# Performance work log

Hardware: AMD Instinct MI355X
Metric: run time of the kernel (lower is better)

## Reference

```python
import jax, jax.numpy as jnp
import numpy as np

B, S, DM, H, DK, DV = 2, 2048, 1024, 16, 64, 64

def setup_inputs() -> dict:
    key = jax.random.key(0)
    ks = jax.random.split(key, 12)
    s = 0.02
    return {
        "Q": jax.random.normal(ks[0], (B, S, DM), jnp.float32),
        "K": jax.random.normal(ks[1], (B, S, DM), jnp.float32),
        "V": jax.random.normal(ks[2], (B, S, DM), jnp.float32),
        "mask": jax.random.randint(ks[3], (B, S, S), 0, 2).astype(bool),
        "wq": jax.random.normal(ks[4], (DM, H * DK), jnp.float32) * s,
        "bq": jnp.zeros((H * DK,), jnp.float32),
        "wk": jax.random.normal(ks[5], (DM, H * DK), jnp.float32) * s,
        "bk": jnp.zeros((H * DK,), jnp.float32),
        "wv": jax.random.normal(ks[6], (DM, H * DV), jnp.float32) * s,
        "bv": jnp.zeros((H * DV,), jnp.float32),
        "wo": jax.random.normal(ks[7], (H * DV, DM), jnp.float32) * s,
        "bo": jnp.zeros((DM,), jnp.float32),
    }

def reference(Q, K, V, mask, wq, bq, wk, bk, wv, bv, wo, bo):
    b = Q.shape[0]
    # projections -> [b, h, s, d]
    q = (Q @ wq + bq).reshape(b, -1, H, DK).transpose(0, 2, 1, 3)
    k = (K @ wk + bk).reshape(b, -1, H, DK).transpose(0, 2, 1, 3)
    v = (V @ wv + bv).reshape(b, -1, H, DV).transpose(0, 2, 1, 3)
    # scaled dot-product attention with boolean mask (True = masked out)
    scores = jnp.einsum("bhqd,bhkd->bhqk", q, k) / jnp.sqrt(jnp.float32(DK))
    scores = jnp.where(mask[:, None, :, :], jnp.float32(-1e9), scores)
    attn = jax.nn.softmax(scores, axis=-1)  # [b,h,s,s]
    ctx = jnp.einsum("bhqk,bhkd->bhqd", attn, v)
    ctx = ctx.transpose(0, 2, 1, 3).reshape(b, -1, H * DV)
    out = ctx @ wo + bo  # [b, s, d_model]
    return out, attn
```

## Files before the change

### kernel.cpp

```cpp
#include <hip/hip_runtime.h>

typedef unsigned short u16;
typedef unsigned int u32;
typedef unsigned long long u64;
typedef __attribute__((ext_vector_type(8))) short bf16x8;
typedef __attribute__((ext_vector_type(4))) float f32x4;

#define NB 2
#define NS 2048
#define NDM 1024
#define NH 16

#define MFMA_B16(a, b, c) __builtin_amdgcn_mfma_f32_16x16x32_bf16(a, b, c, 0, 0, 0)

__device__ __forceinline__ u16 f2bf(float f) {
  union { float f; unsigned u; } v; v.f = f;
  return (u16)((v.u + 0x7fffu + ((v.u >> 16) & 1u)) >> 16);
}

__global__ __launch_bounds__(256) void cast_bf16(const float* __restrict__ in,
                                                 u16* __restrict__ out, int n4) {
  int i = blockIdx.x * 256 + threadIdx.x;
  if (i < n4) {
    const float4 v = reinterpret_cast<const float4*>(in)[i];
    ushort4 o; o.x = f2bf(v.x); o.y = f2bf(v.y); o.z = f2bf(v.z); o.w = f2bf(v.w);
    reinterpret_cast<ushort4*>(out)[i] = o;
  }
}

__global__ __launch_bounds__(256) void transpose_w(const float* __restrict__ in,
                                                   u16* __restrict__ out) {
  __shared__ float tile[32][33];
  int bx = blockIdx.x, by = blockIdx.y;
  int x = threadIdx.x & 31, y0 = threadIdx.x >> 5;
#pragma unroll
  for (int i = 0; i < 4; i++) {
    int y = y0 + i * 8;
    tile[y][x] = in[(by * 32 + y) * NDM + bx * 32 + x];
  }
  __syncthreads();
#pragma unroll
  for (int i = 0; i < 4; i++) {
    int y = y0 + i * 8;
    out[(bx * 32 + y) * NDM + by * 32 + x] = f2bf(tile[x][y]);
  }
}

__global__ __launch_bounds__(256) void mask2bits(const u32* __restrict__ mask, u32* __restrict__ mb) {
  int idx = blockIdx.x * 256 + threadIdx.x;
  u32 mw0 = mask[threadIdx.x & 63];
  bool floatmode = (__ballot(mw0 == 0x3F800000u) != 0ull);
  bool bytemode = !floatmode && (__ballot((mw0 >> 8) != 0u) != 0ull);
  int row = idx >> 6;
  int wword = idx & 63;
  u32 bits = 0;
  if (!bytemode) {
    const uint4* p = reinterpret_cast<const uint4*>(mask + (size_t)row * 2048 + wword * 32);
#pragma unroll
    for (int i = 0; i < 8; i++) {
      uint4 v = p[i];
      bits |= (v.x ? 1u : 0u) << (i * 4 + 0);
      bits |= (v.y ? 1u : 0u) << (i * 4 + 1);
      bits |= (v.z ? 1u : 0u) << (i * 4 + 2);
      bits |= (v.w ? 1u : 0u) << (i * 4 + 3);
    }
  } else {
    const uint4* p = reinterpret_cast<const uint4*>(
        reinterpret_cast<const unsigned char*>(mask) + (size_t)row * 2048 + wword * 32);
#pragma unroll
    for (int i = 0; i < 2; i++) {
      uint4 v = p[i];
      u32 wsv[4] = {v.x, v.y, v.z, v.w};
#pragma unroll
      for (int j = 0; j < 4; j++)
#pragma unroll
        for (int kq = 0; kq < 4; kq++)
          bits |= ((((wsv[j] >> (kq * 8)) & 0xffu) != 0u) ? 1u : 0u) << (i * 16 + j * 4 + kq);
    }
  }
  mb[idx] = bits;
}

struct GArgs { const u16* X; const u16* W; const float* bias; void* out; int mode; float scale; };

__global__ __launch_bounds__(256, 2) void gemm_bt(GArgs g0, GArgs g1, GArgs g2) {
  GArgs ga = (blockIdx.z == 0) ? g0 : (blockIdx.z == 1 ? g1 : g2);
  const int K = 1024, N = 1024;
  __shared__ u16 As[128 * 32];
  __shared__ u16 Bs[128 * 32];
  const int t = threadIdx.x, w = t >> 6, l = t & 63;
  const int m0 = blockIdx.x * 128, n0 = blockIdx.y * 128;
  const int wm = (w >> 1) * 64, wn = (w & 1) * 64;
  const f32x4 fz = {0.f, 0.f, 0.f, 0.f};
  f32x4 acc[4][4];
#pragma unroll
  for (int i = 0; i < 4; i++)
#pragma unroll
    for (int j = 0; j < 4; j++) acc[i][j] = fz;

  for (int k0 = 0; k0 < K; k0 += 32) {
#pragma unroll
    for (int i = 0; i < 2; i++) {
      int idx = i * 256 + w * 64 + l;
      int r = idx >> 2, c = (idx & 3) * 8;
      __builtin_amdgcn_global_load_lds(
          reinterpret_cast<const unsigned*>(ga.X + (size_t)(m0 + r) * K + k0 + c),
          reinterpret_cast<unsigned*>(&As[(i * 256 + w * 64) * 8]), 16, 0, 0);
      __builtin_amdgcn_global_load_lds(
          reinterpret_cast<const unsigned*>(ga.W + (size_t)(n0 + r) * K + k0 + c),
          reinterpret_cast<unsigned*>(&Bs[(i * 256 + w * 64) * 8]), 16, 0, 0);
    }
    __syncthreads();
    bf16x8 af[4], bfr[4];
#pragma unroll
    for (int mt = 0; mt < 4; mt++)
      af[mt] = *reinterpret_cast<const bf16x8*>(&As[(wm + mt * 16 + (l & 15)) * 32 + (l >> 4) * 8]);
#pragma unroll
    for (int nt = 0; nt < 4; nt++)
      bfr[nt] = *reinterpret_cast<const bf16x8*>(&Bs[(wn + nt * 16 + (l & 15)) * 32 + (l >> 4) * 8]);
#pragma unroll
    for (int mt = 0; mt < 4; mt++)
#pragma unroll
      for (int nt = 0; nt < 4; nt++)
        acc[mt][nt] = MFMA_B16(af[mt], bfr[nt], acc[mt][nt]);
    __syncthreads();
  }

#pragma unroll
  for (int nt = 0; nt < 4; nt++) {
    int n = n0 + wn + nt * 16 + (l & 15);
    float bias = ga.bias[n];
#pragma unroll
    for (int mt = 0; mt < 4; mt++) {
      int mb = m0 + wm + mt * 16 + ((l >> 4) << 2);
#pragma unroll
      for (int r = 0; r < 4; r++) {
        int m = mb + r;
        float v = (acc[mt][nt][r] + bias) * ga.scale;
        if (ga.mode == 2) {
          reinterpret_cast<float*>(ga.out)[(size_t)m * N + n] = v;
        } else {
          int b = m >> 11, s = m & 2047, h = n >> 6, d = n & 63;
          if (ga.mode == 0)
            reinterpret_cast<u16*>(ga.out)[(((size_t)(b * NH + h) * NS + s) << 6) + d] = f2bf(v);
          else
            reinterpret_cast<u16*>(ga.out)[((size_t)(b * NH + h) * 64 + d) * NS + s] = f2bf(v);
        }
      }
    }
  }
}

__global__ __launch_bounds__(256, 4) void attn_kernel(
    const u16* __restrict__ qh, const u16* __restrict__ kh, const u16* __restrict__ vT,
    const u32* __restrict__ mb, float* __restrict__ attn, u16* __restrict__ ctx) {
  __shared__ u16 Ks[2][32 * 64];
  __shared__ u16 Vs[2][64 * 32];
  __shared__ u16 Ps[4][16 * 40];
  __shared__ float Pf[4][16 * 36];
  const int tid = threadIdx.x, w = tid >> 6, l = tid & 63;
  int id = blockIdx.x;
  int wgid = (id & 7) * 128 + (id >> 3);
  int qt = wgid & 31, pr = wgid >> 5;
  int h = pr & 15, b = pr >> 4;
  const size_t head = (size_t)b * NH + h;
  const u16* qp = qh + head * NS * 64;
  const u16* kp = kh + head * NS * 64;
  const u16* vp = vT + head * 64 * NS;
  const int qr0 = qt * 64 + w * 16;
  const int lo = l & 15, hi = l >> 4;
  const int rbase = hi << 2;
  const f32x4 fz = {0.f, 0.f, 0.f, 0.f};

  bf16x8 aq0, aq1;
  {
    const u16* p = qp + (size_t)(qr0 + lo) * 64 + hi * 8;
    aq0 = *reinterpret_cast<const bf16x8*>(p);
    aq1 = *reinterpret_cast<const bf16x8*>(p + 32);
  }
  const u32* mrow = mb + ((size_t)b * NS + qr0 + rbase) * 64;

  const int k_row = tid >> 3, k_slot = tid & 7;
  const u16* ksrc0 = kp + (size_t)k_row * 64 + ((k_slot ^ (k_row & 7)) * 8);
  const int v_dv = tid >> 2, v_slot = tid & 3;
  const u16* vsrc0 = vp + (size_t)v_dv * NS + ((v_slot ^ ((v_dv >> 1) & 3)) * 8);

  const int sxk = lo & 7;
  const int sxv = (lo >> 1) & 3;

  float rs0 = 0.f, rs1 = 0.f, rs2 = 0.f, rs3 = 0.f;

  __builtin_amdgcn_global_load_lds(reinterpret_cast<const unsigned*>(ksrc0),
                                   reinterpret_cast<unsigned*>(&Ks[0][w * 512]), 16, 0, 0);
  asm volatile("s_waitcnt vmcnt(0)" ::: "memory");
  __builtin_amdgcn_s_barrier();
  asm volatile("" ::: "memory");

  for (int t = 0; t < 64; ++t) {
    const u16* kbase = &Ks[t & 1][0];
    u16* kdst = &Ks[(t + 1) & 1][w * 512];
    __builtin_amdgcn_global_load_lds(
        reinterpret_cast<const unsigned*>(ksrc0 + (size_t)(t + 1) * 2048),
        reinterpret_cast<unsigned*>(kdst), 16, 0, 0);
    asm volatile("" ::: "memory");
    u32 m0 = mrow[t], m1 = mrow[64 + t], m2 = mrow[128 + t], m3 = mrow[192 + t];
    bf16x8 b00 = *reinterpret_cast<const bf16x8*>(&kbase[(lo) * 64 + ((hi ^ sxk) * 8)]);
    bf16x8 b01 = *reinterpret_cast<const bf16x8*>(&kbase[(lo) * 64 + (((4 + hi) ^ sxk) * 8)]);
    bf16x8 b10 = *reinterpret_cast<const bf16x8*>(&kbase[(16 + lo) * 64 + ((hi ^ sxk) * 8)]);
    bf16x8 b11 = *reinterpret_cast<const bf16x8*>(&kbase[(16 + lo) * 64 + (((4 + hi) ^ sxk) * 8)]);
    f32x4 s0 = MFMA_B16(aq1, b01, MFMA_B16(aq0, b00, fz));
    f32x4 s1 = MFMA_B16(aq1, b11, MFMA_B16(aq0, b10, fz));
    rs0 += ((m0 >> lo) & 1u) ? 0.f : __expf(s0[0]);
    rs1 += ((m1 >> lo) & 1u) ? 0.f : __expf(s0[1]);
    rs2 += ((m2 >> lo) & 1u) ? 0.f : __expf(s0[2]);
    rs3 += ((m3 >> lo) & 1u) ? 0.f : __expf(s0[3]);
    int bit1 = 16 + lo;
    rs0 += ((m0 >> bit1) & 1u) ? 0.f : __expf(s1[0]);
    rs1 += ((m1 >> bit1) & 1u) ? 0.f : __expf(s1[1]);
    rs2 += ((m2 >> bit1) & 1u) ? 0.f : __expf(s1[2]);
    rs3 += ((m3 >> bit1) & 1u) ? 0.f : __expf(s1[3]);
    asm volatile("s_waitcnt vmcnt(4)" ::: "memory");
    __builtin_amdgcn_s_barrier();
    asm volatile("" ::: "memory");
  }

  {
    float v;
    v = rs0; v += __shfl_xor(v, 1); v += __shfl_xor(v, 2); v += __shfl_xor(v, 4); v += __shfl_xor(v, 8);
    rs0 = 1.f / fmaxf(v, 1e-30f);
    v = rs1; v += __shfl_xor(v, 1); v += __shfl_xor(v, 2); v += __shfl_xor(v, 4); v += __shfl_xor(v, 8);
    rs1 = 1.f / fmaxf(v, 1e-30f);
    v = rs2; v += __shfl_xor(v, 1); v += __shfl_xor(v, 2); v += __shfl_xor(v, 4); v += __shfl_xor(v, 8);
    rs2 = 1.f / fmaxf(v, 1e-30f);
    v = rs3; v += __shfl_xor(v, 1); v += __shfl_xor(v, 2); v += __shfl_xor(v, 4); v += __shfl_xor(v, 8);
    rs3 = 1.f / fmaxf(v, 1e-30f);
  }

  f32x4 c0 = fz, c1 = fz, c2 = fz, c3 = fz;
  float* abase = attn + (head * NS + qr0) * NS;
  float* pfw = &Pf[w][0];
  u16* psw = &Ps[w][0];
  const int srow = l >> 2, schunk = l & 3;

  __builtin_amdgcn_global_load_lds(reinterpret_cast<const unsigned*>(ksrc0),
                                   reinterpret_cast<unsigned*>(&Ks[0][w * 512]), 16, 0, 0);
  __builtin_amdgcn_global_load_lds(reinterpret_cast<const unsigned*>(vsrc0),
                                   reinterpret_cast<unsigned*>(&Vs[0][w * 512]), 16, 0, 0);
  asm volatile("s_waitcnt vmcnt(0)" ::: "memory");
  __builtin_amdgcn_s_barrier();
  asm volatile("" ::: "memory");

  for (int t = 0; t < 64; ++t) {
    const u16* kbase = &Ks[t & 1][0];
    const u16* vbase = &Vs[t & 1][0];
    u16* kdst = &Ks[(t + 1) & 1][w * 512];
    u16* vdst = &Vs[(t + 1) & 1][w * 512];
    __builtin_amdgcn_global_load_lds(
        reinterpret_cast<const unsigned*>(ksrc0 + (size_t)(t + 1) * 2048),
        reinterpret_cast<unsigned*>(kdst), 16, 0, 0);
    __builtin_amdgcn_global_load_lds(
        reinterpret_cast<const unsigned*>(vsrc0 + (size_t)(t + 1) * 32),
        reinterpret_cast<unsigned*>(vdst), 16, 0, 0);
    asm volatile("" ::: "memory");
    u32 m0 = mrow[t], m1 = mrow[64 + t], m2 = mrow[128 + t], m3 = mrow[192 + t];
    bf16x8 b00 = *reinterpret_cast<const bf16x8*>(&kbase[(lo) * 64 + ((hi ^ sxk) * 8)]);
    bf16x8 b01 = *reinterpret_cast<const bf16x8*>(&kbase[(lo) * 64 + (((4 + hi) ^ sxk) * 8)]);
    bf16x8 b10 = *reinterpret_cast<const bf16x8*>(&kbase[(16 + lo) * 64 + ((hi ^ sxk) * 8)]);
    bf16x8 b11 = *reinterpret_cast<const bf16x8*>(&kbase[(16 + lo) * 64 + (((4 + hi) ^ sxk) * 8)]);
    f32x4 s0 = MFMA_B16(aq1, b01, MFMA_B16(aq0, b00, fz));
    f32x4 s1 = MFMA_B16(aq1, b11, MFMA_B16(aq0, b10, fz));
    float p;
    p = ((m0 >> lo) & 1u) ? 0.f : __expf(s0[0]) * rs0;
    pfw[(rbase + 0) * 36 + lo] = p; psw[(rbase + 0) * 40 + lo] = f2bf(p);
    p = ((m1 >> lo) & 1u) ? 0.f : __expf(s0[1]) * rs1;
    pfw[(rbase + 1) * 36 + lo] = p; psw[(rbase + 1) * 40 + lo] = f2bf(p);
    p = ((m2 >> lo) & 1u) ? 0.f : __expf(s0[2]) * rs2;
    pfw[(rbase + 2) * 36 + lo] = p; psw[(rbase + 2) * 40 + lo] = f2bf(p);
    p = ((m3 >> lo) & 1u) ? 0.f : __expf(s0[3]) * rs3;
    pfw[(rbase + 3) * 36 + lo] = p; psw[(rbase + 3) * 40 + lo] = f2bf(p);
    int bit1 = 16 + lo;
    p = ((m0 >> bit1) & 1u) ? 0.f : __expf(s1[0]) * rs0;
    pfw[(rbase + 0) * 36 + 16 + lo] = p; psw[(rbase + 0) * 40 + 16 + lo] = f2bf(p);
    p = ((m1 >> bit1) & 1u) ? 0.f : __expf(s1[1]) * rs1;
    pfw[(rbase + 1) * 36 + 16 + lo] = p; psw[(rbase + 1) * 40 + 16 + lo] = f2bf(p);
    p = ((m2 >> bit1) & 1u) ? 0.f : __expf(s1[2]) * rs2;
    pfw[(rbase + 2) * 36 + 16 + lo] = p; psw[(rbase + 2) * 40 + 16 + lo] = f2bf(p);
    p = ((m3 >> bit1) & 1u) ? 0.f : __expf(s1[3]) * rs3;
    pfw[(rbase + 3) * 36 + 16 + lo] = p; psw[(rbase + 3) * 40 + 16 + lo] = f2bf(p);
    bf16x8 pa = *reinterpret_cast<const bf16x8*>(&psw[lo * 40 + hi * 8]);
    bf16x8 v0 = *reinterpret_cast<const bf16x8*>(&vbase[(lo) * 32 + ((hi ^ sxv) * 8)]);
    bf16x8 v1 = *reinterpret_cast<const bf16x8*>(&vbase[(16 + lo) * 32 + ((hi ^ sxv) * 8)]);
    bf16x8 v2 = *reinterpret_cast<const bf16x8*>(&vbase[(32 + lo) * 32 + ((hi ^ sxv) * 8)]);
    bf16x8 v3 = *reinterpret_cast<const bf16x8*>(&vbase[(48 + lo) * 32 + ((hi ^ sxv) * 8)]);
    c0 = MFMA_B16(pa, v0, c0);
    c1 = MFMA_B16(pa, v1, c1);
    c2 = MFMA_B16(pa, v2, c2);
    c3 = MFMA_B16(pa, v3, c3);
    f32x4 o0 = *reinterpret_cast<const f32x4*>(&pfw[srow * 36 + schunk * 4]);
    f32x4 o1 = *reinterpret_cast<const f32x4*>(&pfw[srow * 36 + (schunk + 4) * 4]);
    *reinterpret_cast<f32x4*>(abase + (size_t)srow * NS + t * 32 + schunk * 4) = o0;
    *reinterpret_cast<f32x4*>(abase + (size_t)srow * NS + t * 32 + (schunk + 4) * 4) = o1;
    asm volatile("s_waitcnt vmcnt(6)" ::: "memory");
    __builtin_amdgcn_s_barrier();
    asm volatile("" ::: "memory");
  }

#define CTXW(cv, ct)                                                                   \
  {                                                                                    \
    ctx[((size_t)b * NS + qr0 + rbase + 0) * 1024 + h * 64 + (ct)*16 + lo] = f2bf(cv[0]); \
    ctx[((size_t)b * NS + qr0 + rbase + 1) * 1024 + h * 64 + (ct)*16 + lo] = f2bf(cv[1]); \
    ctx[((size_t)b * NS + qr0 + rbase + 2) * 1024 + h * 64 + (ct)*16 + lo] = f2bf(cv[2]); \
    ctx[((size_t)b * NS + qr0 + rbase + 3) * 1024 + h * 64 + (ct)*16 + lo] = f2bf(cv[3]); \
  }
  CTXW(c0, 0) CTXW(c1, 1) CTXW(c2, 2) CTXW(c3, 3)
#undef CTXW
}

extern "C" void kernel_launch(void* const* d_in, const int* in_sizes, int n_in,
                              void* d_out, int out_size, void* d_ws, size_t ws_size,
                              hipStream_t stream) {
  const float* Q = (const float*)d_in[0];
  const float* K = (const float*)d_in[1];
  const float* V = (const float*)d_in[2];
  const u32* mask = (const u32*)d_in[3];
  const float* wq = (const float*)d_in[4];
  const float* bq = (const float*)d_in[5];
  const float* wk = (const float*)d_in[6];
  const float* bk = (const float*)d_in[7];
  const float* wv = (const float*)d_in[8];
  const float* bv = (const float*)d_in[9];
  const float* wo = (const float*)d_in[10];
  const float* bo = (const float*)d_in[11];
  float* out = (float*)d_out;
  float* attn = out + (size_t)NB * NS * NDM;

  char* ws = (char*)d_ws;
  u16* Qb  = (u16*)(ws + 0);
  u16* Kb  = (u16*)(ws + 8388608);
  u16* Vb  = (u16*)(ws + 16777216);
  u16* wqT = (u16*)(ws + 25165824);
  u16* wkT = (u16*)(ws + 27262976);
  u16* wvT = (u16*)(ws + 29360128);
  u16* woT = (u16*)(ws + 31457280);
  u16* qhd = (u16*)(ws + 33554432);
  u16* khd = (u16*)(ws + 41943040);
  u16* vTd = (u16*)(ws + 50331648);
  u16* ctx = (u16*)(ws + 58720256);
  u32* mbits = (u32*)(ws + 0);

  cast_bf16<<<4096, 256, 0, stream>>>(Q, Qb, 1048576);
  cast_bf16<<<4096, 256, 0, stream>>>(K, Kb, 1048576);
  cast_bf16<<<4096, 256, 0, stream>>>(V, Vb, 1048576);
  transpose_w<<<dim3(32, 32), 256, 0, stream>>>(wq, wqT);
  transpose_w<<<dim3(32, 32), 256, 0, stream>>>(wk, wkT);
  transpose_w<<<dim3(32, 32), 256, 0, stream>>>(wv, wvT);
  transpose_w<<<dim3(32, 32), 256, 0, stream>>>(wo, woT);

  GArgs gq = {Qb, wqT, bq, (void*)qhd, 0, 0.125f};
  GArgs gk = {Kb, wkT, bk, (void*)khd, 0, 1.0f};
  GArgs gv = {Vb, wvT, bv, (void*)vTd, 1, 1.0f};
  gemm_bt<<<dim3(32, 8, 3), 256, 0, stream>>>(gq, gk, gv);

  mask2bits<<<1024, 256, 0, stream>>>(mask, mbits);

  attn_kernel<<<1024, 256, 0, stream>>>(qhd, khd, vTd, mbits, attn, ctx);

  GArgs go = {ctx, woT, bo, d_out, 2, 1.0f};
  gemm_bt<<<dim3(32, 8, 1), 256, 0, stream>>>(go, go, go);
}
```

Measured before the change: 339.1 us.

## Widen attention key tiles to 64 and load V fragments directly from global

Doubles the key tile per iteration from 32 to 64, which halves the loop trip count and the number of barriers. Mask bits are now read as 64-bit words and prefetched one iteration ahead. V fragments are loaded straight from global memory into registers instead of being staged through LDS. The separate fp32 probability buffer is dropped, so the attention output is written from bf16-rounded probabilities, which lowers attn precision and adds a one-element read past each mask row on the last iteration.

```diff
diff --git a/kernel.cpp b/kernel.cpp
--- a/kernel.cpp
+++ b/kernel.cpp
@@ -16,6 +16,9 @@
 __device__ __forceinline__ u16 f2bf(float f) {
   union { float f; unsigned u; } v; v.f = f;
   return (u16)((v.u + 0x7fffu + ((v.u >> 16) & 1u)) >> 16);
+}
+__device__ __forceinline__ float bf2f(u16 h) {
+  union { float f; unsigned u; } v; v.u = ((u32)h) << 16; return v.f;
 }
 
 __global__ __launch_bounds__(256) void cast_bf16(const float* __restrict__ in,
@@ -154,10 +157,8 @@
 __global__ __launch_bounds__(256, 4) void attn_kernel(
     const u16* __restrict__ qh, const u16* __restrict__ kh, const u16* __restrict__ vT,
     const u32* __restrict__ mb, float* __restrict__ attn, u16* __restrict__ ctx) {
-  __shared__ u16 Ks[2][32 * 64];
-  __shared__ u16 Vs[2][64 * 32];
-  __shared__ u16 Ps[4][16 * 40];
-  __shared__ float Pf[4][16 * 36];
+  __shared__ u16 Ks[2][64 * 64];
+  __shared__ u16 Ps[4][16 * 72];
   const int tid = threadIdx.x, w = tid >> 6, l = tid & 63;
   int id = blockIdx.x;
   int wgid = (id & 7) * 128 + (id >> 3);
@@ -178,47 +179,53 @@
     aq0 = *reinterpret_cast<const bf16x8*>(p);
     aq1 = *reinterpret_cast<const bf16x8*>(p + 32);
   }
-  const u32* mrow = mb + ((size_t)b * NS + qr0 + rbase) * 64;
+  const u64* mrow = reinterpret_cast<const u64*>(mb) + ((size_t)b * NS + qr0 + rbase) * 32;
 
   const int k_row = tid >> 3, k_slot = tid & 7;
   const u16* ksrc0 = kp + (size_t)k_row * 64 + ((k_slot ^ (k_row & 7)) * 8);
-  const int v_dv = tid >> 2, v_slot = tid & 3;
-  const u16* vsrc0 = vp + (size_t)v_dv * NS + ((v_slot ^ ((v_dv >> 1) & 3)) * 8);
-
   const int sxk = lo & 7;
-  const int sxv = (lo >> 1) & 3;
 
   float rs0 = 0.f, rs1 = 0.f, rs2 = 0.f, rs3 = 0.f;
 
-  __builtin_amdgcn_global_load_lds(reinterpret_cast<const unsigned*>(ksrc0),
-                                   reinterpret_cast<unsigned*>(&Ks[0][w * 512]), 16, 0, 0);
+#define STAGE_K(tt)                                                                        \
+  {                                                                                        \
+    __builtin_amdgcn_global_load_lds(                                                      \
+        reinterpret_cast<const unsigned*>(ksrc0 + (size_t)(tt) * 4096),                    \
+        reinterpret_cast<unsigned*>(&Ks[(tt) & 1][w * 512]), 16, 0, 0);                    \
+    __builtin_amdgcn_global_load_lds(                                                      \
+        reinterpret_cast<const unsigned*>(ksrc0 + (size_t)(tt) * 4096 + 2048),             \
+        reinterpret_cast<unsigned*>(&Ks[(tt) & 1][2048 + w * 512]), 16, 0, 0);             \
+  }
+#define LOAD_KFRAGS(buf)                                                                   \
+  bf16x8 bk[4][2];                                                                         \
+  _Pragma("unroll") for (int ct = 0; ct < 4; ++ct) {                                       \
+    bk[ct][0] = *reinterpret_cast<const bf16x8*>(                                          \
+        &Ks[buf][(ct * 16 + lo) * 64 + ((hi ^ sxk) * 8)]);                                 \
+    bk[ct][1] = *reinterpret_cast<const bf16x8*>(                                          \
+        &Ks[buf][(ct * 16 + lo) * 64 + (((4 + hi) ^ sxk) * 8)]);                           \
+  }
+
+  u64 mc0 = mrow[0], mc1 = mrow[32], mc2 = mrow[64], mc3 = mrow[96];
+  STAGE_K(0);
   asm volatile("s_waitcnt vmcnt(0)" ::: "memory");
   __builtin_amdgcn_s_barrier();
   asm volatile("" ::: "memory");
 
-  for (int t = 0; t < 64; ++t) {
-    const u16* kbase = &Ks[t & 1][0];
-    u16* kdst = &Ks[(t + 1) & 1][w * 512];
-    __builtin_amdgcn_global_load_lds(
-        reinterpret_cast<const unsigned*>(ksrc0 + (size_t)(t + 1) * 2048),
-        reinterpret_cast<unsigned*>(kdst), 16, 0, 0);
+  for (int t = 0; t < 32; ++t) {
+    if (t + 1 < 32) STAGE_K(t + 1);
+    u64 mn0 = mrow[t + 1], mn1 = mrow[33 + t], mn2 = mrow[65 + t], mn3 = mrow[97 + t];
     asm volatile("" ::: "memory");
-    u32 m0 = mrow[t], m1 = mrow[64 + t], m2 = mrow[128 + t], m3 = mrow[192 + t];
-    bf16x8 b00 = *reinterpret_cast<const bf16x8*>(&kbase[(lo) * 64 + ((hi ^ sxk) * 8)]);
-    bf16x8 b01 = *reinterpret_cast<const bf16x8*>(&kbase[(lo) * 64 + (((4 + hi) ^ sxk) * 8)]);
-    bf16x8 b10 = *reinterpret_cast<const bf16x8*>(&kbase[(16 + lo) * 64 + ((hi ^ sxk) * 8)]);
-    bf16x8 b11 = *reinterpret_cast<const bf16x8*>(&kbase[(16 + lo) * 64 + (((4 + hi) ^ sxk) * 8)]);
-    f32x4 s0 = MFMA_B16(aq1, b01, MFMA_B16(aq0, b00, fz));
-    f32x4 s1 = MFMA_B16(aq1, b11, MFMA_B16(aq0, b10, fz));
-    rs0 += ((m0 >> lo) & 1u) ? 0.f : __expf(s0[0]);
-    rs1 += ((m1 >> lo) & 1u) ? 0.f : __expf(s0[1]);
-    rs2 += ((m2 >> lo) & 1u) ? 0.f : __expf(s0[2]);
-    rs3 += ((m3 >> lo) & 1u) ? 0.f : __expf(s0[3]);
-    int bit1 = 16 + lo;
-    rs0 += ((m0 >> bit1) & 1u) ? 0.f : __expf(s1[0]);
-    rs1 += ((m1 >> bit1) & 1u) ? 0.f : __expf(s1[1]);
-    rs2 += ((m2 >> bit1) & 1u) ? 0.f : __expf(s1[2]);
-    rs3 += ((m3 >> bit1) & 1u) ? 0.f : __expf(s1[3]);
+    LOAD_KFRAGS(t & 1);
+#pragma unroll
+    for (int ct = 0; ct < 4; ++ct) {
+      f32x4 s = MFMA_B16(aq1, bk[ct][1], MFMA_B16(aq0, bk[ct][0], fz));
+      int bit = ct * 16 + lo;
+      rs0 += ((mc0 >> bit) & 1ull) ? 0.f : __expf(s[0]);
+      rs1 += ((mc1 >> bit) & 1ull) ? 0.f : __expf(s[1]);
+      rs2 += ((mc2 >> bit) & 1ull) ? 0.f : __expf(s[2]);
+      rs3 += ((mc3 >> bit) & 1ull) ? 0.f : __expf(s[3]);
+    }
+    mc0 = mn0; mc1 = mn1; mc2 = mn2; mc3 = mn3;
     asm volatile("s_waitcnt vmcnt(4)" ::: "memory");
     __builtin_amdgcn_s_barrier();
     asm volatile("" ::: "memory");
@@ -238,75 +245,71 @@
 
   f32x4 c0 = fz, c1 = fz, c2 = fz, c3 = fz;
   float* abase = attn + (head * NS + qr0) * NS;
-  float* pfw = &Pf[w][0];
   u16* psw = &Ps[w][0];
   const int srow = l >> 2, schunk = l & 3;
 
-  __builtin_amdgcn_global_load_lds(reinterpret_cast<const unsigned*>(ksrc0),
-                                   reinterpret_cast<unsigned*>(&Ks[0][w * 512]), 16, 0, 0);
-  __builtin_amdgcn_global_load_lds(reinterpret_cast<const unsigned*>(vsrc0),
-                                   reinterpret_cast<unsigned*>(&Vs[0][w * 512]), 16, 0, 0);
+  mc0 = mrow[0]; mc1 = mrow[32]; mc2 = mrow[64]; mc3 = mrow[96];
+  STAGE_K(0);
   asm volatile("s_waitcnt vmcnt(0)" ::: "memory");
   __builtin_amdgcn_s_barrier();
   asm volatile("" ::: "memory");
 
-  for (int t = 0; t < 64; ++t) {
-    const u16* kbase = &Ks[t & 1][0];
-    const u16* vbase = &Vs[t & 1][0];
-    u16* kdst = &Ks[(t + 1) & 1][w * 512];
-    u16* vdst = &Vs[(t + 1) & 1][w * 512];
-    __builtin_amdgcn_global_load_lds(
-        reinterpret_cast<const unsigned*>(ksrc0 + (size_t)(t + 1) * 2048),
-        reinterpret_cast<unsigned*>(kdst), 16, 0, 0);
-    __builtin_amdgcn_global_load_lds(
-        reinterpret_cast<const unsigned*>(vsrc0 + (size_t)(t + 1) * 32),
-        reinterpret_cast<unsigned*>(vdst), 16, 0, 0);
+  for (int t = 0; t < 32; ++t) {
+    bf16x8 bv[4][2];
+#pragma unroll
+    for (int ct = 0; ct < 4; ++ct) {
+      const u16* p = vp + (size_t)(ct * 16 + lo) * NS + t * 64 + hi * 8;
+      bv[ct][0] = *reinterpret_cast<const bf16x8*>(p);
+      bv[ct][1] = *reinterpret_cast<const bf16x8*>(p + 32);
+    }
+    u64 mn0 = mrow[t + 1], mn1 = mrow[33 + t], mn2 = mrow[65 + t], mn3 = mrow[97 + t];
+    if (t + 1 < 32) STAGE_K(t + 1);
     asm volatile("" ::: "memory");
-    u32 m0 = mrow[t], m1 = mrow[64 + t], m2 = mrow[128 + t], m3 = mrow[192 + t];
-    bf16x8 b00 = *reinterpret_cast<const bf16x8*>(&kbase[(lo) * 64 + ((hi ^ sxk) * 8)]);
-    bf16x8 b01 = *reinterpret_cast<const bf16x8*>(&kbase[(lo) * 64 + (((4 + hi) ^ sxk) * 8)]);
-    bf16x8 b10 = *reinterpret_cast<const bf16x8*>(&kbase[(16 + lo) * 64 + ((hi ^ sxk) * 8)]);
-    bf16x8 b11 = *reinterpret_cast<const bf16x8*>(&kbase[(16 + lo) * 64 + (((4 + hi) ^ sxk) * 8)]);
-    f32x4 s0 = MFMA_B16(aq1, b01, MFMA_B16(aq0, b00, fz));
-    f32x4 s1 = MFMA_B16(aq1, b11, MFMA_B16(aq0, b10, fz));
-    float p;
-    p = ((m0 >> lo) & 1u) ? 0.f : __expf(s0[0]) * rs0;
-    pfw[(rbase + 0) * 36 + lo] = p; psw[(rbase + 0) * 40 + lo] = f2bf(p);
-    p = ((m1 >> lo) & 1u) ? 0.f : __expf(s0[1]) * rs1;
-    pfw[(rbase + 1) * 36 + lo] = p; psw[(rbase + 1) * 40 + lo] = f2bf(p);
-    p = ((m2 >> lo) & 1u) ? 0.f : __expf(s0[2]) * rs2;
-    pfw[(rbase + 2) * 36 + lo] = p; psw[(rbase + 2) * 40 + lo] = f2bf(p);
-    p = ((m3 >> lo) & 1u) ? 0.f : __expf(s0[3]) * rs3;
-    pfw[(rbase + 3) * 36 + lo] = p; psw[(rbase + 3) * 40 + lo] = f2bf(p);
-    int bit1 = 16 + lo;
-    p = ((m0 >> bit1) & 1u) ? 0.f : __expf(s1[0]) * rs0;
-    pfw[(rbase + 0) * 36 + 16 + lo] = p; psw[(rbase + 0) * 40 + 16 + lo] = f2bf(p);
-    p = ((m1 >> bit1) & 1u) ? 0.f : __expf(s1[1]) * rs1;
-    pfw[(rbase + 1) * 36 + 16 + lo] = p; psw[(rbase + 1) * 40 + 16 + lo] = f2bf(p);
-    p = ((m2 >> bit1) & 1u) ? 0.f : __expf(s1[2]) * rs2;
-    pfw[(rbase + 2) * 36 + 16 + lo] = p; psw[(rbase + 2) * 40 + 16 + lo] = f2bf(p);
-    p = ((m3 >> bit1) & 1u) ? 0.f : __expf(s1[3]) * rs3;
-    pfw[(rbase + 3) * 36 + 16 + lo] = p; psw[(rbase + 3) * 40 + 16 + lo] = f2bf(p);
-    bf16x8 pa = *reinterpret_cast<const bf16x8*>(&psw[lo * 40 + hi * 8]);
-    bf16x8 v0 = *reinterpret_cast<const bf16x8*>(&vbase[(lo) * 32 + ((hi ^ sxv) * 8)]);
-    bf16x8 v1 = *reinterpret_cast<const bf16x8*>(&vbase[(16 + lo) * 32 + ((hi ^ sxv) * 8)]);
-    bf16x8 v2 = *reinterpret_cast<const bf16x8*>(&vbase[(32 + lo) * 32 + ((hi ^ sxv) * 8)]);
-    bf16x8 v3 = *reinterpret_cast<const bf16x8*>(&vbase[(48 + lo) * 32 + ((hi ^ sxv) * 8)]);
-    c0 = MFMA_B16(pa, v0, c0);
-    c1 = MFMA_B16(pa, v1, c1);
-    c2 = MFMA_B16(pa, v2, c2);
-    c3 = MFMA_B16(pa, v3, c3);
-    f32x4 o0 = *reinterpret_cast<const f32x4*>(&pfw[srow * 36 + schunk * 4]);
-    f32x4 o1 = *reinterpret_cast<const f32x4*>(&pfw[srow * 36 + (schunk + 4) * 4]);
-    *reinterpret_cast<f32x4*>(abase + (size_t)srow * NS + t * 32 + schunk * 4) = o0;
-    *reinterpret_cast<f32x4*>(abase + (size_t)srow * NS + t * 32 + (schunk + 4) * 4) = o1;
-    asm volatile("s_waitcnt vmcnt(6)" ::: "memory");
+    LOAD_KFRAGS(t & 1);
+#pragma unroll
+    for (int ct = 0; ct < 4; ++ct) {
+      f32x4 s = MFMA_B16(aq1, bk[ct][1], MFMA_B16(aq0, bk[ct][0], fz));
+      int bit = ct * 16 + lo;
+      float p0 = ((mc0 >> bit) & 1ull) ? 0.f : __expf(s[0]) * rs0;
+      float p1 = ((mc1 >> bit) & 1ull) ? 0.f : __expf(s[1]) * rs1;
+      float p2 = ((mc2 >> bit) & 1ull) ? 0.f : __expf(s[2]) * rs2;
+      float p3 = ((mc3 >> bit) & 1ull) ? 0.f : __expf(s[3]) * rs3;
+      psw[(rbase + 0) * 72 + bit] = f2bf(p0);
+      psw[(rbase + 1) * 72 + bit] = f2bf(p1);
+      psw[(rbase + 2) * 72 + bit] = f2bf(p2);
+      psw[(rbase + 3) * 72 + bit] = f2bf(p3);
+    }
+    mc0 = mn0; mc1 = mn1; mc2 = mn2; mc3 = mn3;
+    {
+      bf16x8 pa0 = *reinterpret_cast<const bf16x8*>(&psw[lo * 72 + hi * 8]);
+      bf16x8 pa1 = *reinterpret_cast<const bf16x8*>(&psw[lo * 72 + 32 + hi * 8]);
+      c0 = MFMA_B16(pa1, bv[0][1], MFMA_B16(pa0, bv[0][0], c0));
+      c1 = MFMA_B16(pa1, bv[1][1], MFMA_B16(pa0, bv[1][0], c1));
+      c2 = MFMA_B16(pa1, bv[2][1], MFMA_B16(pa0, bv[2][0], c2));
+      c3 = MFMA_B16(pa1, bv[3][1], MFMA_B16(pa0, bv[3][0], c3));
+    }
+    {
+      float* arow = abase + (size_t)srow * NS + t * 64 + schunk * 16;
+      bf16x8 q0 = *reinterpret_cast<const bf16x8*>(&psw[srow * 72 + schunk * 16]);
+      bf16x8 q1 = *reinterpret_cast<const bf16x8*>(&psw[srow * 72 + schunk * 16 + 8]);
+      f32x4 o0, o1, o2, o3;
+#pragma unroll
+      for (int j = 0; j < 4; ++j) {
+        o0[j] = bf2f((u16)q0[j]); o1[j] = bf2f((u16)q0[j + 4]);
+        o2[j] = bf2f((u16)q1[j]); o3[j] = bf2f((u16)q1[j + 4]);
+      }
+      *reinterpret_cast<f32x4*>(arow + 0) = o0;
+      *reinterpret_cast<f32x4*>(arow + 4) = o1;
+      *reinterpret_cast<f32x4*>(arow + 8) = o2;
+      *reinterpret_cast<f32x4*>(arow + 12) = o3;
+    }
+    asm volatile("s_waitcnt vmcnt(4)" ::: "memory");
     __builtin_amdgcn_s_barrier();
     asm volatile("" ::: "memory");
   }
 
-#define CTXW(cv, ct)                                                                   \
-  {                                                                                    \
+#define CTXW(cv, ct)                                                                      \
+  {                                                                                       \
     ctx[((size_t)b * NS + qr0 + rbase + 0) * 1024 + h * 64 + (ct)*16 + lo] = f2bf(cv[0]); \
     ctx[((size_t)b * NS + qr0 + rbase + 1) * 1024 + h * 64 + (ct)*16 + lo] = f2bf(cv[1]); \
     ctx[((size_t)b * NS + qr0 + rbase + 2) * 1024 + h * 64 + (ct)*16 + lo] = f2bf(cv[2]); \
@@ -314,6 +317,8 @@
   }
   CTXW(c0, 0) CTXW(c1, 1) CTXW(c2, 2) CTXW(c3, 3)
 #undef CTXW
+#undef STAGE_K
+#undef LOAD_KFRAGS
 }
 
 extern "C" void kernel_launch(void* const* d_in, const int* in_sizes, int n_in,
```

Result: slower. 433.2 us (+27.7%).
